# Kernel tuning notes

Hardware: AMD Instinct MI355X
Metric: run time of the kernel (lower is better)

Reference implementation:

```python
import jax, jax.numpy as jnp
import numpy as np
from jax import lax

TAU = 0.3
K_TOP = 1
_EPS = 1e-5


def _epcor(src, tgt, src_emb, tgt_emb):
    # src/tgt: (B,3,N)/(B,3,M); src_emb/tgt_emb: (B,C,N)/(B,C,M)
    B, _, N = src.shape
    M = tgt.shape[2]
    src_K = int(N * TAU)
    tgt_K = int(M * TAU)

    # negative squared distance: -||s||^2 + 2 s.t - ||t||^2
    xx = jnp.sum(src_emb ** 2, axis=1)            # (B,N)
    yy = jnp.sum(tgt_emb ** 2, axis=1)            # (B,M)
    pd = (2.0 * jnp.einsum('bcn,bcm->bnm', src_emb, tgt_emb)
          - xx[:, :, None] - yy[:, None, :])      # (B,N,M)

    ssc = jax.nn.softmax(pd, axis=2)              # row softmax (B,N,M)
    col_sum = jnp.sum(ssc, axis=1, keepdims=True) # (B,1,M)
    kth_col = -lax.top_k(-col_sum, tgt_K)[0][..., -1:]  # tgt_K-th smallest (B,1,1)
    mask_tgt = col_sum < kth_col                  # (B,1,M)

    ssr = jax.nn.softmax(pd, axis=1)              # col softmax
    row_sum = jnp.sum(ssr, axis=2, keepdims=True) # (B,N,1)
    kth_row = -lax.top_k(-row_sum[..., 0], src_K)[0][:, -1]  # (B,)
    mask_src = row_sum < kth_row[:, None, None]   # (B,N,1)

    mask = jnp.logical_or(mask_src, mask_tgt)     # (B,N,M)
    row_max = lax.top_k(ssc, K_TOP)[0][..., -1:]  # K-th largest per row (B,N,1)
    # faithful to torch: (mask + scoresSoftCol) < topk  (bool + float adds 1.0)
    mask2 = (mask.astype(pd.dtype) + ssc) < row_max

    sparse = jnp.where(mask2, 0.0, ssc)
    col_sum_sp = jnp.sum(sparse, axis=-1, keepdims=True)
    col_sum_sp = jnp.where(col_sum_sp < _EPS, _EPS, col_sum_sp)
    w = sparse / col_sum_sp                       # (B,N,M) renormalized weights

    val_sum = jnp.sum(w, axis=-1, keepdims=True)  # (B,N,1)
    vsi = jnp.where(mask_src, 0.0, val_sum)[..., 0]  # (B,N)
    src_weight = vsi / jnp.sum(vsi, axis=-1, keepdims=True)

    src_corr = jnp.einsum('bcm,bnm->bcn', tgt, w)  # (B,3,N)
    return src_corr, src_weight, mask_src, mask_tgt


def _svd_weighted(src, src_corr, weights):
    a = jnp.swapaxes(src, -1, -2)        # (B,N,3)
    b = jnp.swapaxes(src_corr, -1, -2)   # (B,N,3)
    wn = weights[..., None] / (jnp.sum(weights[..., None], axis=1, keepdims=True) + _EPS)
    ca = jnp.sum(a * wn, axis=1)         # (B,3)
    cb = jnp.sum(b * wn, axis=1)
    ac = a - ca[:, None, :]
    bc = b - cb[:, None, :]
    cov = jnp.einsum('bnd,bne->bde', ac, bc * wn)  # (B,3,3)
    u, s, vh = jnp.linalg.svd(cov)
    v = jnp.swapaxes(vh, -1, -2)
    ut = jnp.swapaxes(u, -1, -2)
    rot_pos = v @ ut
    v_neg = v.at[:, :, 2].multiply(-1.0)
    rot_neg = v_neg @ ut
    rot = jnp.where(jnp.linalg.det(rot_pos)[:, None, None] > 0, rot_pos, rot_neg)
    trans = (-rot @ ca[..., None] + cb[..., None])[..., 0]  # (B,3)
    return rot, trans


def setup_inputs() -> dict:
    key = jax.random.key(0)
    k1, k2, k3, k4 = jax.random.split(key, 4)
    B, C, N = 8, 512, 2048
    return {
        'src': jax.random.normal(k1, (B, 3, N), dtype=jnp.float32),
        'tgt': jax.random.normal(k2, (B, 3, N), dtype=jnp.float32),
        'src_emb': jax.random.normal(k3, (B, C, N), dtype=jnp.float32) * 0.05,
        'tgt_emb': jax.random.normal(k4, (B, C, N), dtype=jnp.float32) * 0.05,
    }


def reference(src, tgt, src_emb, tgt_emb):
    src_corr, src_weight, mask_src, mask_tgt = _epcor(src, tgt, src_emb, tgt_emb)
    # original wraps SVD in torch.no_grad()
    rot, trans = _svd_weighted(lax.stop_gradient(src),
                               lax.stop_gradient(src_corr),
                               lax.stop_gradient(src_weight))
    return src_corr, src_weight, mask_src, mask_tgt, rot, trans
```

## Files before the change

kernel.cpp:

```cpp
#include <hip/hip_runtime.h>
#include <math.h>

#define B_ 8
#define C_ 512
#define N_ 2048
#define M_ 2048
#define KSEL 614
#define EPS_ 1e-5f
#define CS_ 8

#define O_CORR 0
#define O_W    (B_*3*N_)
#define O_MSRC (O_W + B_*N_)
#define O_MTGT (O_MSRC + B_*N_)
#define O_ROT  (O_MTGT + B_*M_)
#define O_TR   (O_ROT + B_*9)

typedef short bf16x8 __attribute__((ext_vector_type(8)));
typedef float f32x4 __attribute__((ext_vector_type(4)));

__device__ inline unsigned short f2bf(float f){
  unsigned u = __float_as_uint(f);
  return (unsigned short)((u + 0x7FFFu + ((u >> 16) & 1u)) >> 16);
}
__device__ inline float bf2f(unsigned short h){
  return __uint_as_float(((unsigned)h) << 16);
}

__device__ inline double blk_sumd(double v, double* sh){
  int t = threadIdx.x;
  sh[t] = v; __syncthreads();
  for (int s = 128; s > 0; s >>= 1) { if (t < s) sh[t] += sh[t+s]; __syncthreads(); }
  double r = sh[0]; __syncthreads(); return r;
}

__global__ __launch_bounds__(256) void ksqcomb(const float* __restrict__ partA,
                                               const float* __restrict__ partB,
                                               float* __restrict__ xx,
                                               float* __restrict__ yy)
{
  int i = blockIdx.x*256 + threadIdx.x;
  const float* part = blockIdx.y ? partB : partA;
  float* out = blockIdx.y ? yy : xx;
  float s = 0.f;
  for (int cs = 0; cs < CS_; ++cs) s += part[(size_t)cs*B_*N_ + i];
  out[i] = s;
}

__global__ __launch_bounds__(256) void ksplit(const float* __restrict__ XA,
                                              const float* __restrict__ XB,
                                              unsigned short* __restrict__ XhA,
                                              unsigned short* __restrict__ XlA,
                                              unsigned short* __restrict__ XhB,
                                              unsigned short* __restrict__ XlB,
                                              float* __restrict__ sqpartA,
                                              float* __restrict__ sqpartB)
{
  __shared__ float tile[64][65];
  int p0 = blockIdx.x*64, c0 = blockIdx.y*64;
  int zb = blockIdx.z;
  int b = zb & (B_-1);
  int side = zb >> 3;
  const float* X = side ? XB : XA;
  unsigned short* Xh = side ? XhB : XhA;
  unsigned short* Xl = side ? XlB : XlA;
  float* sqpart = side ? sqpartB : sqpartA;
  int cs = blockIdx.y;
  int t = threadIdx.x;
  const float* base = X + ((size_t)b*C_ + c0)*N_ + p0;
  int px = (t & 15)*4, cy = t >> 4;
#pragma unroll
  for (int i = 0; i < 4; ++i) {
    int c = cy + i*16;
    float4 v = *(const float4*)(base + (size_t)c*N_ + px);
    tile[px+0][c] = v.x; tile[px+1][c] = v.y; tile[px+2][c] = v.z; tile[px+3][c] = v.w;
  }
  __syncthreads();
  int cx = (t & 15)*4, py = t >> 4;
  unsigned short* oh = Xh + ((size_t)b*N_ + p0)*C_ + c0;
  unsigned short* ol = Xl + ((size_t)b*N_ + p0)*C_ + c0;
#pragma unroll
  for (int i = 0; i < 4; ++i) {
    int p = py + i*16;
    float v0 = tile[p][cx], v1 = tile[p][cx+1], v2 = tile[p][cx+2], v3 = tile[p][cx+3];
    ushort4 h, l;
    h.x = f2bf(v0); l.x = f2bf(v0 - bf2f(h.x));
    h.y = f2bf(v1); l.y = f2bf(v1 - bf2f(h.y));
    h.z = f2bf(v2); l.z = f2bf(v2 - bf2f(h.z));
    h.w = f2bf(v3); l.w = f2bf(v3 - bf2f(h.w));
    *(ushort4*)(oh + (size_t)p*C_ + cx) = h;
    *(ushort4*)(ol + (size_t)p*C_ + cx) = l;
    float sqv = v0*v0 + v1*v1 + v2*v2 + v3*v3;
#pragma unroll
    for (int off = 1; off < 16; off <<= 1) sqv += __shfl_xor(sqv, off, 16);
    if ((t & 15) == 0) sqpart[((size_t)cs*B_ + b)*N_ + p0 + p] = sqv;
  }
}

__global__ __launch_bounds__(256, 1) void kgemm_mfma(
    const unsigned short* __restrict__ Ahg, const unsigned short* __restrict__ Alg,
    const unsigned short* __restrict__ Bhg, const unsigned short* __restrict__ Blg,
    const float* __restrict__ xx, const float* __restrict__ yy,
    float* __restrict__ E, float* __restrict__ rowps, float* __restrict__ rowpm,
    float* __restrict__ colps, int b_off)
{
  __shared__ unsigned short smem[2*4*128*32];

  int sflat = blockIdx.x + 16*blockIdx.y;
  int xcd = sflat & 7, si = sflat >> 3;
  int ka = xcd >> 1, kb = xcd & 1;
  int bn = ka*4 + (si & 3);
  int bm = kb*8 + (si >> 2);
  int bz = blockIdx.z;
  int b = b_off + bz;
  int t = threadIdx.x;
  int lane = t & 63, w = t >> 6;
  int wr = (w >> 1)*64, wc = (w & 1)*64;
  int lrow = lane & 15, lgr = (lane >> 4)*8;
  size_t abase = ((size_t)b*N_ + (size_t)bn*128)*C_;
  size_t bbase = ((size_t)b*M_ + (size_t)bm*128)*C_;
  int lr4 = lane >> 2;
  int lc4s = ((lane & 3)*8) ^ (((lr4 >> 1) & 3) << 3);
  int lgr_sw = lgr ^ (((lrow >> 1) & 3) << 3);

  f32x4 acc[4][4];
#pragma unroll
  for (int i = 0; i < 4; ++i)
#pragma unroll
    for (int j = 0; j < 4; ++j) acc[i][j] = (f32x4){0.f, 0.f, 0.f, 0.f};

#define ISSUE(bufk, K0) do { \
    unsigned short* bb0 = smem + (bufk)*16384; \
    _Pragma("unroll") \
    for (int q = 0; q < 2; ++q) { \
      int rblk = w*2 + q; \
      size_t roff = (size_t)(rblk*16 + lr4)*C_ + (K0) + lc4s; \
      unsigned short* ldsb = bb0 + rblk*512; \
      __builtin_amdgcn_global_load_lds((const void*)(Ahg + abase + roff), (void*)(ldsb),         16, 0, 0); \
      __builtin_amdgcn_global_load_lds((const void*)(Alg + abase + roff), (void*)(ldsb + 4096),  16, 0, 0); \
      __builtin_amdgcn_global_load_lds((const void*)(Bhg + bbase + roff), (void*)(ldsb + 8192),  16, 0, 0); \
      __builtin_amdgcn_global_load_lds((const void*)(Blg + bbase + roff), (void*)(ldsb + 12288), 16, 0, 0); \
    } \
  } while (0)

  ISSUE(0, 0);
  int cur = 0;
  for (int ks = 0; ks < 16; ++ks) {
    __syncthreads();
    if (ks < 15) { int k0n = (ks+1)*32; ISSUE(cur^1, k0n); }
    unsigned short* bb = smem + cur*16384;
    unsigned short* Ahs = bb;
    unsigned short* Als = bb + 4096;
    unsigned short* Bhs = bb + 8192;
    unsigned short* Bls = bb + 12288;
    bf16x8 ah[4], al[4], bh[4], bl[4];
#pragma unroll
    for (int f = 0; f < 4; ++f) {
      int ra = (wr + f*16 + lrow)*32 + lgr_sw;
      int rb = (wc + f*16 + lrow)*32 + lgr_sw;
      ah[f] = *(const bf16x8*)&Ahs[ra];
      al[f] = *(const bf16x8*)&Als[ra];
      bh[f] = *(const bf16x8*)&Bhs[rb];
      bl[f] = *(const bf16x8*)&Bls[rb];
    }
#pragma unroll
    for (int fi = 0; fi < 4; ++fi)
#pragma unroll
      for (int fj = 0; fj < 4; ++fj) {
        acc[fi][fj] = __builtin_amdgcn_mfma_f32_16x16x32_bf16(ah[fi], bh[fj], acc[fi][fj], 0, 0, 0);
        acc[fi][fj] = __builtin_amdgcn_mfma_f32_16x16x32_bf16(ah[fi], bl[fj], acc[fi][fj], 0, 0, 0);
        acc[fi][fj] = __builtin_amdgcn_mfma_f32_16x16x32_bf16(al[fi], bh[fj], acc[fi][fj], 0, 0, 0);
      }
    cur ^= 1;
  }
#undef ISSUE

  float* eps = (float*)smem;
  float* Eb = E + (size_t)bz*N_*M_;
  int lg = lane >> 4;
  int row0 = t >> 5;
  int c4 = (t & 31)*4;
  const float* yb = yy + b*M_ + bm*128;
  float4 vy = *(const float4*)(yb + c4);
  float ca0 = 0.f, ca1 = 0.f, ca2 = 0.f, ca3 = 0.f;
#pragma unroll
  for (int pass = 0; pass < 2; ++pass) {
    __syncthreads();
    if ((w >> 1) == pass) {
#pragma unroll
      for (int fi = 0; fi < 4; ++fi) {
        int nl = lg*4 + fi*16;
#pragma unroll
        for (int fj = 0; fj < 4; ++fj) {
          int ml = wc + (lane & 15) + fj*16;
#pragma unroll
          for (int r = 0; r < 4; ++r)
            eps[(nl + r)*132 + ml] = acc[fi][fj][r];
        }
      }
    }
    __syncthreads();
#pragma unroll
    for (int it = 0; it < 8; ++it) {
      int row = it*8 + row0;
      int gn = bn*128 + pass*64 + row;
      float xv = xx[b*N_ + gn];
      float4 s = *(float4*)&eps[row*132 + c4];
      float4 o;
      o.x = expf(2.f*s.x - xv - vy.x);
      o.y = expf(2.f*s.y - xv - vy.y);
      o.z = expf(2.f*s.z - xv - vy.z);
      o.w = expf(2.f*s.w - xv - vy.w);
      *(float4*)(Eb + (size_t)gn*M_ + bm*128 + c4) = o;
      float rs = o.x + o.y + o.z + o.w;
      float rm2 = fmaxf(fmaxf(o.x, o.y), fmaxf(o.z, o.w));
      ca0 += o.x; ca1 += o.y; ca2 += o.z; ca3 += o.w;
#pragma unroll
      for (int off = 16; off > 0; off >>= 1) {
        rs += __shfl_xor(rs, off, 32);
        rm2 = fmaxf(rm2, __shfl_xor(rm2, off, 32));
      }
      if ((t & 31) == 0) {
        rowps[(size_t)bm*B_*N_ + (size_t)b*N_ + gn] = rs;
        rowpm[(size_t)bm*B_*N_ + (size_t)b*N_ + gn] = rm2;
      }
    }
  }
  __syncthreads();
  float* colsh = (float*)smem;
  colsh[row0*128 + c4+0] = ca0;
  colsh[row0*128 + c4+1] = ca1;
  colsh[row0*128 + c4+2] = ca2;
  colsh[row0*128 + c4+3] = ca3;
  __syncthreads();
  if (t < 128) {
    float s = 0.f;
#pragma unroll
    for (int g = 0; g < 8; ++g) s += colsh[g*128 + t];
    colps[(size_t)bn*B_*M_ + (size_t)b*M_ + bm*128 + t] = s;
  }
}

__global__ __launch_bounds__(256) void kstatcomb(
    const float* __restrict__ rowps, const float* __restrict__ rowpm,
    const float* __restrict__ colps,
    float* __restrict__ rowZf, float* __restrict__ rowSmax,
    float* __restrict__ colZ0f, int b_off)
{
  int i = blockIdx.x*256 + threadIdx.x;
  size_t gi = (size_t)b_off*N_ + i;
  if (blockIdx.y == 0) {
    double s = 0.0; float mx = 0.f;
#pragma unroll
    for (int k = 0; k < 16; ++k) {
      s += (double)rowps[(size_t)k*B_*N_ + gi];
      mx = fmaxf(mx, rowpm[(size_t)k*B_*N_ + gi]);
    }
    float zf = (float)s;
    rowZf[gi] = zf;
    rowSmax[gi] = mx * (1.f / zf);
  } else {
    double s = 0.0;
#pragma unroll
    for (int k = 0; k < 16; ++k) s += (double)colps[(size_t)k*B_*M_ + gi];
    colZ0f[gi] = (float)s;
  }
}

__global__ __launch_bounds__(256) void kcross(const float* __restrict__ E,
                                              const float* __restrict__ rowZf,
                                              const float* __restrict__ colZ0f,
                                              double* __restrict__ colSp,
                                              double* __restrict__ rowSp, int b_off)
{
  __shared__ float tile[64*129];
  __shared__ double rzinv[64];
  __shared__ double czinv[128];
  __shared__ double shd[256];
  int rc = blockIdx.x, cc = blockIdx.y, bz = blockIdx.z;
  int b = b_off + bz;
  int r0 = rc*64, c0 = cc*128;
  int t = threadIdx.x;
  const float* Eb = E + (size_t)bz*N_*M_;
  {
    int rr = t >> 5, cq = (t & 31)*4;
#pragma unroll
    for (int it = 0; it < 8; ++it) {
      int row = it*8 + rr;
      float4 v = *(const float4*)(Eb + (size_t)(r0+row)*M_ + c0 + cq);
      tile[row*129 + cq+0] = v.x;
      tile[row*129 + cq+1] = v.y;
      tile[row*129 + cq+2] = v.z;
      tile[row*129 + cq+3] = v.w;
    }
  }
  if (t < 64) rzinv[t] = 1.0 / (double)rowZf[(size_t)b*N_ + r0 + t];
  if (t >= 128) czinv[t-128] = 1.0 / (double)colZ0f[(size_t)b*M_ + c0 + (t-128)];
  __syncthreads();
  {
    int j = t & 127, rg = t >> 7;
    double a = 0.0;
    for (int rr = rg*32; rr < rg*32 + 32; ++rr)
      a += (double)tile[rr*129 + j] * rzinv[rr];
    shd[rg*128 + j] = a;
  }
  __syncthreads();
  if (t < 128)
    colSp[(size_t)rc*B_*M_ + (size_t)b*M_ + c0 + t] = shd[t] + shd[128 + t];
  __syncthreads();
  {
    int r = t & 63, h = t >> 6;
    double a = 0.0;
    for (int j = h*32; j < h*32 + 32; ++j)
      a += (double)tile[r*129 + j] * czinv[j];
    shd[h*64 + r] = a;
  }
  __syncthreads();
  if (t < 64)
    rowSp[(size_t)cc*B_*N_ + (size_t)b*N_ + r0 + t] = shd[t] + shd[64+t] + shd[128+t] + shd[192+t];
}

__global__ __launch_bounds__(256) void kcombab(const double* __restrict__ colSp,
                                               const double* __restrict__ rowSp,
                                               double* __restrict__ col_sum,
                                               double* __restrict__ row_sum, int b_off)
{
  int i = blockIdx.x*256 + threadIdx.x;
  if (blockIdx.y == 0) {
    size_t gi = (size_t)b_off*M_ + i;
    double s = 0.0;
    for (int k = 0; k < 32; ++k) s += colSp[(size_t)k*B_*M_ + gi];
    col_sum[gi] = s;
  } else {
    size_t gi = (size_t)b_off*N_ + i;
    double s = 0.0;
    for (int k = 0; k < 16; ++k) s += rowSp[(size_t)k*B_*N_ + gi];
    row_sum[gi] = s;
  }
}

__global__ __launch_bounds__(256) void kkth(const double* __restrict__ col_sum,
                                            const double* __restrict__ row_sum,
                                            double* __restrict__ kth_c,
                                            double* __restrict__ kth_r, int b_off)
{
  __shared__ double sv[2048];
  int b = b_off + blockIdx.y;
  const double* v = (blockIdx.z == 0 ? col_sum : row_sum) + b*2048;
  double* kth = (blockIdx.z == 0 ? kth_c : kth_r);
  int t = threadIdx.x;
  for (int i = t; i < 2048; i += 256) sv[i] = v[i];
  __syncthreads();
  int i = blockIdx.x*256 + t;
  double vi = sv[i];
  int lt = 0, le = 0;
  for (int j = 0; j < 2048; ++j) { double vj = sv[j]; lt += (vj < vi); le += (vj <= vi); }
  if (lt < KSEL && KSEL <= le) kth[b] = vi;
}

__global__ __launch_bounds__(256) void kmask(const double* __restrict__ col_sum,
                                             const double* __restrict__ row_sum,
                                             const double* __restrict__ kth_c,
                                             const double* __restrict__ kth_r,
                                             unsigned char* __restrict__ colmask,
                                             unsigned char* __restrict__ rowmask,
                                             float* __restrict__ out, int b_off)
{
  int side = blockIdx.y;
  const double* vals = side ? row_sum : col_sum;
  const double* kth = side ? kth_r : kth_c;
  unsigned char* m8 = side ? rowmask : colmask;
  float* mout = out + (side ? O_MSRC : O_MTGT);
  int i = blockIdx.x*256 + threadIdx.x;
  int b = b_off + i/2048, j = i & 2047;
  bool m = vals[b*2048 + j] < kth[b];
  m8[b*2048 + j] = m ? 1 : 0;
  mout[b*2048 + j] = m ? 1.f : 0.f;
}

__global__ __launch_bounds__(256) void kwcorr(
    const float* __restrict__ E, const float* __restrict__ rowZf,
    const float* __restrict__ rowSmax,
    const unsigned char* __restrict__ rowmask, const unsigned char* __restrict__ colmask,
    const float* __restrict__ tgt, float* __restrict__ vsi,
    float* __restrict__ corrf, float* __restrict__ corr_out, int b_off)
{
  __shared__ float shred[20];
  int r = blockIdx.x, t = threadIdx.x;
  int bz = r / N_, n = r % N_;
  int b = b_off + bz;
  const float* row = E + (size_t)bz*N_*M_ + (size_t)n*M_;
  float rinv = 1.f / rowZf[b*N_+n];
  int lane = t & 63, w = t >> 6;
  float rmax = rowSmax[b*N_+n];
  int rm = rowmask[b*N_+n];
  const unsigned char* cm = colmask + b*M_;
  float v[8];
  unsigned kp = 0;
  float s = 0.f;
#pragma unroll
  for (int il = 0; il < 8; ++il) {
    int m = t + il*256;
    float vv = row[m] * rinv;
    v[il] = vv;
    bool keep = rm || cm[m] || (vv >= rmax);
    kp |= (keep ? 1u : 0u) << il;
    if (keep) s += vv;
  }
#pragma unroll
  for (int off = 32; off; off >>= 1) s += __shfl_xor(s, off, 64);
  if (!lane) shred[w] = s;
  __syncthreads();
  s = shred[0] + shred[1] + shred[2] + shred[3];
  float d = (s < EPS_) ? EPS_ : s;
  float dinv = 1.f / d;
  const float* t0 = tgt + (size_t)b*3*M_;
  float vs = 0.f, a0 = 0.f, a1 = 0.f, a2 = 0.f;
#pragma unroll
  for (int il = 0; il < 8; ++il) {
    int m = t + il*256;
    float wv = (kp >> il & 1u) ? v[il]*dinv : 0.f;
    vs += wv;
    a0 += wv * t0[m];
    a1 += wv * t0[M_+m];
    a2 += wv * t0[2*M_+m];
  }
#pragma unroll
  for (int off = 32; off; off >>= 1) {
    vs += __shfl_xor(vs, off, 64);
    a0 += __shfl_xor(a0, off, 64);
    a1 += __shfl_xor(a1, off, 64);
    a2 += __shfl_xor(a2, off, 64);
  }
  if (!lane) {
    shred[4 + w] = vs; shred[8 + w] = a0; shred[12 + w] = a1; shred[16 + w] = a2;
  }
  __syncthreads();
  if (!t) {
    float vsT = shred[4]+shred[5]+shred[6]+shred[7];
    float a0T = shred[8]+shred[9]+shred[10]+shred[11];
    float a1T = shred[12]+shred[13]+shred[14]+shred[15];
    float a2T = shred[16]+shred[17]+shred[18]+shred[19];
    vsi[b*N_+n] = rm ? 0.f : vsT;
    size_t o = (size_t)b*3*N_ + n;
    corrf[o] = a0T; corrf[o+N_] = a1T; corrf[o+2*N_] = a2T;
    corr_out[o]      = a0T;
    corr_out[o+N_]   = a1T;
    corr_out[o+2*N_] = a2T;
  }
}

__global__ __launch_bounds__(256) void ksumvsi(const float* __restrict__ vsi,
                                               float* __restrict__ out)
{
  __shared__ double shd[256];
  int b = blockIdx.x;
  double s = 0.0;
  for (int n = threadIdx.x; n < N_; n += 256) s += (double)vsi[b*N_+n];
  s = blk_sumd(s, shd);
  if (!threadIdx.x) out[b] = (float)s;
}

__global__ __launch_bounds__(256) void kweights(const float* __restrict__ vsi,
                                                const float* __restrict__ sumvsi,
                                                float* __restrict__ srcw,
                                                float* __restrict__ wout)
{
  int i = blockIdx.x*256 + threadIdx.x;
  if (i >= B_*N_) return;
  int b = i / N_;
  float w = vsi[i] / sumvsi[b];
  srcw[i] = w;
  wout[i] = w;
}

__global__ __launch_bounds__(256) void kcov(const float* __restrict__ srcw,
                                            const float* __restrict__ src,
                                            const float* __restrict__ corrf,
                                            double* covd, double* cad, double* cbd)
{
  __shared__ double sh[256];
  int b = blockIdx.x, t = threadIdx.x;
  const float* w = srcw + b*N_;
  const float* a = src  + (size_t)b*3*N_;
  const float* bb = corrf + (size_t)b*3*N_;
  double sw = 0.0;
  for (int n = t; n < N_; n += 256) sw += (double)w[n];
  sw = blk_sumd(sw, sh);
  double inv = 1.0/(sw + 1e-5);
  double p0=0,p1=0,p2=0,p3=0,p4=0,p5=0;
  for (int n = t; n < N_; n += 256) {
    double wn = (double)w[n]*inv;
    p0 += (double)a[n]*wn;      p1 += (double)a[N_+n]*wn;   p2 += (double)a[2*N_+n]*wn;
    p3 += (double)bb[n]*wn;     p4 += (double)bb[N_+n]*wn;  p5 += (double)bb[2*N_+n]*wn;
  }
  double ca0 = blk_sumd(p0, sh), ca1 = blk_sumd(p1, sh), ca2 = blk_sumd(p2, sh);
  double cb0 = blk_sumd(p3, sh), cb1 = blk_sumd(p4, sh), cb2 = blk_sumd(p5, sh);
  double c[9] = {0,0,0,0,0,0,0,0,0};
  for (int n = t; n < N_; n += 256) {
    double wn = (double)w[n]*inv;
    double a0 = (double)a[n]-ca0, a1d = (double)a[N_+n]-ca1, a2d = (double)a[2*N_+n]-ca2;
    double b0 = ((double)bb[n]-cb0)*wn, b1 = ((double)bb[N_+n]-cb1)*wn, b2 = ((double)bb[2*N_+n]-cb2)*wn;
    c[0]+=a0*b0; c[1]+=a0*b1; c[2]+=a0*b2;
    c[3]+=a1d*b0; c[4]+=a1d*b1; c[5]+=a1d*b2;
    c[6]+=a2d*b0; c[7]+=a2d*b1; c[8]+=a2d*b2;
  }
  for (int k = 0; k < 9; ++k) {
    double rr = blk_sumd(c[k], sh);
    if (!t) covd[b*9+k] = rr;
  }
  if (!t) {
    cad[b*3+0]=ca0; cad[b*3+1]=ca1; cad[b*3+2]=ca2;
    cbd[b*3+0]=cb0; cbd[b*3+1]=cb1; cbd[b*3+2]=cb2;
  }
}

__global__ void ksvd(const double* __restrict__ covd, const double* __restrict__ cad,
                     const double* __restrict__ cbd, float* out)
{
  int b = threadIdx.x;
  if (b >= B_) return;
  double H[3][3];
  for (int i = 0; i < 3; ++i) for (int j = 0; j < 3; ++j) H[i][j] = covd[b*9+i*3+j];
  double A[3][3];
  for (int i = 0; i < 3; ++i)
    for (int j = 0; j < 3; ++j) {
      double s = 0.0;
      for (int l = 0; l < 3; ++l) s += H[l][i]*H[l][j];
      A[i][j] = s;
    }
  double V[3][3] = {{1,0,0},{0,1,0},{0,0,1}};
  const int PP[3] = {0,0,1}, QQ[3] = {1,2,2};
  for (int sweep = 0; sweep < 24; ++sweep) {
    double off = fabs(A[0][1])+fabs(A[0][2])+fabs(A[1][2]);
    if (off < 1e-28) break;
    for (int r = 0; r < 3; ++r) {
      int p = PP[r], q = QQ[r];
      double apq = A[p][q];
      if (fabs(apq) < 1e-300) continue;
      double th = (A[q][q]-A[p][p])/(2.0*apq);
      double tt = (th >= 0.0 ? 1.0 : -1.0)/(fabs(th)+sqrt(th*th+1.0));
      double cc = 1.0/sqrt(tt*tt+1.0), ss = tt*cc;
      for (int k = 0; k < 3; ++k) {
        double akp = A[k][p], akq = A[k][q];
        A[k][p] = cc*akp - ss*akq; A[k][q] = ss*akp + cc*akq;
      }
      for (int k = 0; k < 3; ++k) {
        double apk = A[p][k], aqk = A[q][k];
        A[p][k] = cc*apk - ss*aqk; A[q][k] = ss*apk + cc*aqk;
      }
      for (int k = 0; k < 3; ++k) {
        double vkp = V[k][p], vkq = V[k][q];
        V[k][p] = cc*vkp - ss*vkq; V[k][q] = ss*vkp + cc*vkq;
      }
    }
  }
  double lam[3] = {A[0][0], A[1][1], A[2][2]};
  int idx[3] = {0,1,2};
  for (int i = 0; i < 2; ++i)
    for (int j = i+1; j < 3; ++j)
      if (lam[idx[j]] > lam[idx[i]]) { int tmp = idx[i]; idx[i] = idx[j]; idx[j] = tmp; }
  double Vs[3][3], sig[3];
  for (int i = 0; i < 3; ++i) {
    for (int k = 0; k < 3; ++k) Vs[k][i] = V[k][idx[i]];
    double l = lam[idx[i]];
    sig[i] = sqrt(l > 0.0 ? l : 0.0);
  }
  double U[3][3];
  for (int i = 0; i < 3; ++i) {
    double inv = sig[i] > 1e-300 ? 1.0/sig[i] : 0.0;
    for (int k = 0; k < 3; ++k) {
      double u = H[k][0]*Vs[0][i] + H[k][1]*Vs[1][i] + H[k][2]*Vs[2][i];
      U[k][i] = u*inv;
    }
  }
  if (sig[2] <= 1e-9*sig[0]) {
    U[0][2] = U[1][0]*U[2][1] - U[2][0]*U[1][1];
    U[1][2] = U[2][0]*U[0][1] - U[0][0]*U[2][1];
    U[2][2] = U[0][0]*U[1][1] - U[1][0]*U[0][1];
  }
  double detH = H[0][0]*(H[1][1]*H[2][2]-H[1][2]*H[2][1])
              - H[0][1]*(H[1][0]*H[2][2]-H[1][2]*H[2][0])
              + H[0][2]*(H[1][0]*H[2][1]-H[1][1]*H[2][0]);
  double s3[3] = {1.0, 1.0, detH > 0.0 ? 1.0 : -1.0};
  double R[3][3];
  for (int d = 0; d < 3; ++d)
    for (int e = 0; e < 3; ++e) {
      double s = 0.0;
      for (int i = 0; i < 3; ++i) s += s3[i]*Vs[d][i]*U[e][i];
      R[d][e] = s;
    }
  double tr[3];
  for (int d = 0; d < 3; ++d)
    tr[d] = cbd[b*3+d] - (R[d][0]*cad[b*3+0] + R[d][1]*cad[b*3+1] + R[d][2]*cad[b*3+2]);
  for (int d = 0; d < 3; ++d)
    for (int e = 0; e < 3; ++e)
      out[O_ROT + b*9 + d*3 + e] = (float)R[d][e];
  for (int d = 0; d < 3; ++d)
    out[O_TR + b*3 + d] = (float)tr[d];
}

__global__ void kfail(float* out, float v) { out[0] = v; }

extern "C" void kernel_launch(void* const* d_in, const int* in_sizes, int n_in,
                              void* d_out, int out_size, void* d_ws, size_t ws_size,
                              hipStream_t stream) {
  float* out = (float*)d_out;
  (void)out_size;

  int i_tgt = 1, i_semb = 2;
  if (n_in == 4 && in_sizes[1] == B_*C_*N_) { i_semb = 1; i_tgt = 2; }
  const float* src  = (const float*)d_in[0];
  const float* tgt  = (const float*)d_in[i_tgt];
  const float* semb = (const float*)d_in[i_semb];
  const float* temb = (const float*)d_in[3];

  char* w = (char*)d_ws;
  auto alloc = [&](size_t bytes) { char* p = w; w += (bytes + 255)/256*256; return p; };
  float*  sqpartA = (float*)alloc((size_t)CS_*B_*N_*4);
  float*  sqpartB = (float*)alloc((size_t)CS_*B_*N_*4);
  float*  xx      = (float*)alloc((size_t)B_*N_*4);
  float*  yy      = (float*)alloc((size_t)B_*M_*4);
  float*  rowZf   = (float*)alloc((size_t)B_*N_*4);
  float*  rowSmax = (float*)alloc((size_t)B_*N_*4);
  float*  colZ0f  = (float*)alloc((size_t)B_*M_*4);
  float*  rowps   = (float*)alloc((size_t)16*B_*N_*4);
  float*  rowpm   = (float*)alloc((size_t)16*B_*N_*4);
  float*  colps   = (float*)alloc((size_t)16*B_*M_*4);
  double* colSp   = (double*)alloc((size_t)32*B_*M_*8);
  double* rowSp   = (double*)alloc((size_t)16*B_*N_*8);
  double* col_sum = (double*)alloc((size_t)B_*M_*8);
  double* row_sum = (double*)alloc((size_t)B_*N_*8);
  double* kth_c   = (double*)alloc((size_t)B_*8);
  double* kth_r   = (double*)alloc((size_t)B_*8);
  unsigned char* rowmask = (unsigned char*)alloc((size_t)B_*N_);
  unsigned char* colmask = (unsigned char*)alloc((size_t)B_*M_);
  float*  vsi     = (float*)alloc((size_t)B_*N_*4);
  float*  srcw    = (float*)alloc((size_t)B_*N_*4);
  float*  sumvsi  = (float*)alloc((size_t)B_*4);
  float*  corrf   = (float*)alloc((size_t)B_*3*N_*4);
  double* covd = (double*)alloc((size_t)B_*9*8);
  double* cad  = (double*)alloc((size_t)B_*3*8);
  double* cbd  = (double*)alloc((size_t)B_*3*8);
  unsigned short* Ahg = (unsigned short*)alloc((size_t)B_*N_*C_*2);
  unsigned short* Alg = (unsigned short*)alloc((size_t)B_*N_*C_*2);
  unsigned short* Bhg = (unsigned short*)alloc((size_t)B_*M_*C_*2);
  unsigned short* Blg = (unsigned short*)alloc((size_t)B_*M_*C_*2);

  size_t used = (size_t)(w - (char*)d_ws);
  size_t rem = ws_size > used ? ws_size - used : 0;
  size_t oneE = (size_t)N_*M_*sizeof(float);
  int bc = (int)(rem / oneE);
  if (bc < 1) { kfail<<<1, 1, 0, stream>>>(out, 32768.f); return; }
  if (bc > B_) bc = B_;
  float* E = (float*)w;

  ksplit<<<dim3(N_/64, C_/64, 2*B_), 256, 0, stream>>>(semb, temb, Ahg, Alg, Bhg, Blg,
                                                       sqpartA, sqpartB);
  ksqcomb<<<dim3((B_*N_)/256, 2), 256, 0, stream>>>(sqpartA, sqpartB, xx, yy);

  for (int b0 = 0; b0 < B_; b0 += bc) {
    int cur = (B_ - b0 < bc) ? (B_ - b0) : bc;
    kgemm_mfma<<<dim3(N_/128, M_/128, cur), 256, 0, stream>>>(Ahg, Alg, Bhg, Blg,
                                                              xx, yy, E, rowps, rowpm, colps, b0);
    kstatcomb<<<dim3(cur*N_/256, 2), 256, 0, stream>>>(rowps, rowpm, colps,
                                                       rowZf, rowSmax, colZ0f, b0);
    kcross   <<<dim3(N_/64, M_/128, cur), 256, 0, stream>>>(E, rowZf, colZ0f, colSp, rowSp, b0);
    kcombab  <<<dim3(cur*M_/256, 2), 256, 0, stream>>>(colSp, rowSp, col_sum, row_sum, b0);
    kkth     <<<dim3(8, cur, 2), 256, 0, stream>>>(col_sum, row_sum, kth_c, kth_r, b0);
    kmask    <<<dim3(cur*8, 2), 256, 0, stream>>>(col_sum, row_sum, kth_c, kth_r,
                                                  colmask, rowmask, out, b0);
    kwcorr   <<<cur*N_, 256, 0, stream>>>(E, rowZf, rowSmax, rowmask, colmask, tgt,
                                          vsi, corrf, out + O_CORR, b0);
  }

  ksumvsi <<<B_, 256, 0, stream>>>(vsi, sumvsi);
  kweights<<<(B_*N_+255)/256, 256, 0, stream>>>(vsi, sumvsi, srcw, out + O_W);
  kcov    <<<B_, 256, 0, stream>>>(srcw, src, corrf, covd, cad, cbd);
  ksvd    <<<1, 64, 0, stream>>>(covd, cad, cbd, out);
}
```

Before: 308.4 us.

## Single-buffer GEMM LDS staging and vectorize kwcorr row loads

```diff
diff --git a/kernel.cpp b/kernel.cpp
--- a/kernel.cpp
+++ b/kernel.cpp
@@ -104,7 +104,7 @@
     float* __restrict__ E, float* __restrict__ rowps, float* __restrict__ rowpm,
     float* __restrict__ colps, int b_off)
 {
-  __shared__ unsigned short smem[2*4*128*32];
+  __shared__ unsigned short smem[4*128*32];
 
   int sflat = blockIdx.x + 16*blockIdx.y;
   int xcd = sflat & 7, si = sflat >> 3;
@@ -129,13 +129,12 @@
 #pragma unroll
     for (int j = 0; j < 4; ++j) acc[i][j] = (f32x4){0.f, 0.f, 0.f, 0.f};
 
-#define ISSUE(bufk, K0) do { \
-    unsigned short* bb0 = smem + (bufk)*16384; \
+#define ISSUE(K0) do { \
     _Pragma("unroll") \
     for (int q = 0; q < 2; ++q) { \
       int rblk = w*2 + q; \
       size_t roff = (size_t)(rblk*16 + lr4)*C_ + (K0) + lc4s; \
-      unsigned short* ldsb = bb0 + rblk*512; \
+      unsigned short* ldsb = smem + rblk*512; \
       __builtin_amdgcn_global_load_lds((const void*)(Ahg + abase + roff), (void*)(ldsb),         16, 0, 0); \
       __builtin_amdgcn_global_load_lds((const void*)(Alg + abase + roff), (void*)(ldsb + 4096),  16, 0, 0); \
       __builtin_amdgcn_global_load_lds((const void*)(Bhg + bbase + roff), (void*)(ldsb + 8192),  16, 0, 0); \
@@ -143,16 +142,13 @@
     } \
   } while (0)
 
-  ISSUE(0, 0);
-  int cur = 0;
+  unsigned short* Ahs = smem;
+  unsigned short* Als = smem + 4096;
+  unsigned short* Bhs = smem + 8192;
+  unsigned short* Bls = smem + 12288;
   for (int ks = 0; ks < 16; ++ks) {
+    ISSUE(ks*32);
     __syncthreads();
-    if (ks < 15) { int k0n = (ks+1)*32; ISSUE(cur^1, k0n); }
-    unsigned short* bb = smem + cur*16384;
-    unsigned short* Ahs = bb;
-    unsigned short* Als = bb + 4096;
-    unsigned short* Bhs = bb + 8192;
-    unsigned short* Bls = bb + 12288;
     bf16x8 ah[4], al[4], bh[4], bl[4];
 #pragma unroll
     for (int f = 0; f < 4; ++f) {
@@ -171,7 +167,7 @@
         acc[fi][fj] = __builtin_amdgcn_mfma_f32_16x16x32_bf16(ah[fi], bl[fj], acc[fi][fj], 0, 0, 0);
         acc[fi][fj] = __builtin_amdgcn_mfma_f32_16x16x32_bf16(al[fi], bh[fj], acc[fi][fj], 0, 0, 0);
       }
-    cur ^= 1;
+    __syncthreads();
   }
 #undef ISSUE
 
@@ -195,7 +191,7 @@
           int ml = wc + (lane & 15) + fj*16;
 #pragma unroll
           for (int r = 0; r < 4; ++r)
-            eps[(nl + r)*132 + ml] = acc[fi][fj][r];
+            eps[(nl + r)*128 + ml] = acc[fi][fj][r];
         }
       }
     }
@@ -205,7 +201,7 @@
       int row = it*8 + row0;
       int gn = bn*128 + pass*64 + row;
       float xv = xx[b*N_ + gn];
-      float4 s = *(float4*)&eps[row*132 + c4];
+      float4 s = *(float4*)&eps[row*128 + c4];
       float4 o;
       o.x = expf(2.f*s.x - xv - vy.x);
       o.y = expf(2.f*s.y - xv - vy.y);
@@ -395,17 +391,25 @@
   float rmax = rowSmax[b*N_+n];
   int rm = rowmask[b*N_+n];
   const unsigned char* cm = colmask + b*M_;
-  float v[8];
+  float v0_, v1_, v2_, v3_, v4_, v5_, v6_, v7_;
   unsigned kp = 0;
   float s = 0.f;
-#pragma unroll
-  for (int il = 0; il < 8; ++il) {
-    int m = t + il*256;
-    float vv = row[m] * rinv;
-    v[il] = vv;
-    bool keep = rm || cm[m] || (vv >= rmax);
-    kp |= (keep ? 1u : 0u) << il;
-    if (keep) s += vv;
+  {
+    int m0 = t*4;
+    float4 e0 = *(const float4*)(row + m0);
+    float4 e1 = *(const float4*)(row + m0 + 1024);
+    v0_ = e0.x*rinv; v1_ = e0.y*rinv; v2_ = e0.z*rinv; v3_ = e0.w*rinv;
+    v4_ = e1.x*rinv; v5_ = e1.y*rinv; v6_ = e1.z*rinv; v7_ = e1.w*rinv;
+    uchar4 c0v = *(const uchar4*)(cm + m0);
+    uchar4 c1v = *(const uchar4*)(cm + m0 + 1024);
+    bool k0 = rm || c0v.x || (v0_ >= rmax); if (k0) { s += v0_; kp |= 1u; }
+    bool k1 = rm || c0v.y || (v1_ >= rmax); if (k1) { s += v1_; kp |= 2u; }
+    bool k2 = rm || c0v.z || (v2_ >= rmax); if (k2) { s += v2_; kp |= 4u; }
+    bool k3 = rm || c0v.w || (v3_ >= rmax); if (k3) { s += v3_; kp |= 8u; }
+    bool k4 = rm || c1v.x || (v4_ >= rmax); if (k4) { s += v4_; kp |= 16u; }
+    bool k5 = rm || c1v.y || (v5_ >= rmax); if (k5) { s += v5_; kp |= 32u; }
+    bool k6 = rm || c1v.z || (v6_ >= rmax); if (k6) { s += v6_; kp |= 64u; }
+    bool k7 = rm || c1v.w || (v7_ >= rmax); if (k7) { s += v7_; kp |= 128u; }
   }
 #pragma unroll
   for (int off = 32; off; off >>= 1) s += __shfl_xor(s, off, 64);
@@ -416,14 +420,30 @@
   float dinv = 1.f / d;
   const float* t0 = tgt + (size_t)b*3*M_;
   float vs = 0.f, a0 = 0.f, a1 = 0.f, a2 = 0.f;
-#pragma unroll
-  for (int il = 0; il < 8; ++il) {
-    int m = t + il*256;
-    float wv = (kp >> il & 1u) ? v[il]*dinv : 0.f;
-    vs += wv;
-    a0 += wv * t0[m];
-    a1 += wv * t0[M_+m];
-    a2 += wv * t0[2*M_+m];
+  {
+    int m0 = t*4;
+    float4 tx0 = *(const float4*)(t0 + m0);
+    float4 ty0 = *(const float4*)(t0 + M_ + m0);
+    float4 tz0 = *(const float4*)(t0 + 2*M_ + m0);
+    float w0 = (kp & 1u)   ? v0_*dinv : 0.f;
+    float w1 = (kp & 2u)   ? v1_*dinv : 0.f;
+    float w2 = (kp & 4u)   ? v2_*dinv : 0.f;
+    float w3 = (kp & 8u)   ? v3_*dinv : 0.f;
+    vs += w0+w1+w2+w3;
+    a0 += w0*tx0.x + w1*tx0.y + w2*tx0.z + w3*tx0.w;
+    a1 += w0*ty0.x + w1*ty0.y + w2*ty0.z + w3*ty0.w;
+    a2 += w0*tz0.x + w1*tz0.y + w2*tz0.z + w3*tz0.w;
+    float4 tx1 = *(const float4*)(t0 + m0 + 1024);
+    float4 ty1 = *(const float4*)(t0 + M_ + m0 + 1024);
+    float4 tz1 = *(const float4*)(t0 + 2*M_ + m0 + 1024);
+    float w4 = (kp & 16u)  ? v4_*dinv : 0.f;
+    float w5 = (kp & 32u)  ? v5_*dinv : 0.f;
+    float w6 = (kp & 64u)  ? v6_*dinv : 0.f;
+    float w7 = (kp & 128u) ? v7_*dinv : 0.f;
+    vs += w4+w5+w6+w7;
+    a0 += w4*tx1.x + w5*tx1.y + w6*tx1.z + w7*tx1.w;
+    a1 += w4*ty1.x + w5*ty1.y + w6*ty1.z + w7*ty1.w;
+    a2 += w4*tz1.x + w5*tz1.y + w6*tz1.z + w7*tz1.w;
   }
 #pragma unroll
   for (int off = 32; off; off >>= 1) {
```

New measurement: 291.7 us. 5.4% less time.
